# Optimization experiments

Measured on AMD Instinct MI355X. Metric: run time of the kernel, lower is better.

## Reference

```python
import jax, jax.numpy as jnp
import numpy as np

B, LS, LH, D1, D2 = 16, 1024, 1024, 1024, 1024


def setup_inputs() -> dict:
    key = jax.random.key(0)
    k1, k2, k3 = jax.random.split(key, 3)
    S = jax.random.normal(k1, (B, LS, D1), dtype=jnp.float32)
    H = jax.random.normal(k2, (B, LH, D2), dtype=jnp.float32)
    pad_mask = jnp.zeros((B, LS, LH), dtype=jnp.float32)  # additive mask
    W_w = jax.random.normal(k3, (D2, D1), dtype=jnp.float32) / np.sqrt(D1)
    W_b = jnp.zeros((D2,), dtype=jnp.float32)
    return {"S": S, "H": H, "pad_mask": pad_mask, "W_w": W_w, "W_b": W_b}


def reference(S, H, pad_mask, W_w, W_b):
    # Linear projection: S_ = S @ W^T + b  -> [B, LS, D2]
    S_ = jnp.einsum('bsd,ed->bse', S, W_w) + W_b
    # Unscaled dot-product scores: [B, LS, LH]
    score = jnp.einsum('bse,bte->bst', S_, H)
    score = score + pad_mask  # additive pad mask
    score = jax.nn.softmax(score, axis=-1)
    # Weighted sum of H: [B, LS, D2]
    out = jnp.einsum('bst,bte->bse', score, H)
    return out
```

## Files before the change

kernel.cpp:

```cpp
#include <hip/hip_runtime.h>
#include <stdint.h>

typedef _Float16 half8 __attribute__((ext_vector_type(8)));
typedef float floatx4 __attribute__((ext_vector_type(4)));

__device__ __forceinline__ uint16_t f16bits(_Float16 h) {
  union { _Float16 f; uint16_t u; } x; x.f = h; return x.u;
}

__device__ __forceinline__ void g2l16(const void* g, void* l) {
  __builtin_amdgcn_global_load_lds((const __attribute__((address_space(1))) void*)g,
                                   (__attribute__((address_space(3))) void*)l,
                                   16, 0, 0);
}

__global__ __launch_bounds__(256) void split_f16_kernel(
    const float* __restrict__ x, uint16_t* __restrict__ hi,
    uint16_t* __restrict__ lo, int n4) {
  int i = blockIdx.x * 256 + threadIdx.x;
  if (i >= n4) return;
  float4 v = ((const float4*)x)[i];
  ushort4 h, l;
  _Float16 a;
  a = (_Float16)v.x; h.x = f16bits(a); l.x = f16bits((_Float16)(v.x - (float)a));
  a = (_Float16)v.y; h.y = f16bits(a); l.y = f16bits((_Float16)(v.y - (float)a));
  a = (_Float16)v.z; h.z = f16bits(a); l.z = f16bits((_Float16)(v.z - (float)a));
  a = (_Float16)v.w; h.w = f16bits(a); l.w = f16bits((_Float16)(v.w - (float)a));
  ((ushort4*)hi)[i] = h;
  ((ushort4*)lo)[i] = l;
}

__global__ __launch_bounds__(256) void split_h_kernel(
    const float* __restrict__ src, uint16_t* __restrict__ hi,
    uint16_t* __restrict__ lo, uint16_t* __restrict__ ht) {
  __shared__ uint16_t tile[64][65];
  const int e0 = blockIdx.x * 64;
  const int t0 = blockIdx.y * 64;
  const size_t bb = (size_t)blockIdx.z << 20;
  const int r = threadIdx.x >> 4;
  const int c = (threadIdx.x & 15) * 4;
#pragma unroll
  for (int it = 0; it < 4; ++it) {
    const int tr = r + it * 16;
    const size_t idx = bb + (size_t)(t0 + tr) * 1024 + e0 + c;
    float4 v = *(const float4*)(src + idx);
    ushort4 h, l;
    _Float16 a;
    a = (_Float16)v.x; h.x = f16bits(a); l.x = f16bits((_Float16)(v.x - (float)a));
    a = (_Float16)v.y; h.y = f16bits(a); l.y = f16bits((_Float16)(v.y - (float)a));
    a = (_Float16)v.z; h.z = f16bits(a); l.z = f16bits((_Float16)(v.z - (float)a));
    a = (_Float16)v.w; h.w = f16bits(a); l.w = f16bits((_Float16)(v.w - (float)a));
    *(ushort4*)(hi + idx) = h;
    *(ushort4*)(lo + idx) = l;
    tile[c + 0][tr] = h.x;
    tile[c + 1][tr] = h.y;
    tile[c + 2][tr] = h.z;
    tile[c + 3][tr] = h.w;
  }
  __syncthreads();
#pragma unroll
  for (int it = 0; it < 4; ++it) {
    const int er = r + it * 16;
    ushort4 o;
    o.x = tile[er][c + 0];
    o.y = tile[er][c + 1];
    o.z = tile[er][c + 2];
    o.w = tile[er][c + 3];
    *(ushort4*)(ht + bb + (size_t)(e0 + er) * 1024 + t0 + c) = o;
  }
}

template <bool SPLIT, int MODE, int GMAP>
__global__ __launch_bounds__(256, 4) void gemm_bt(
    const uint16_t* __restrict__ Ahi, const uint16_t* __restrict__ Alo,
    const uint16_t* __restrict__ Bhi, const uint16_t* __restrict__ Blo,
    uint16_t* __restrict__ Chi, uint16_t* __restrict__ Clo,
    float* __restrict__ Cf, const float* __restrict__ mask,
    const float* __restrict__ bias, int N, int K,
    long batchA, long batchB, long batchC) {
  constexpr int NBUF = SPLIT ? 2 : 1;
  constexpr int LOI = SPLIT ? 1 : 0;
  __shared__ __align__(16) uint16_t sA[NBUF][128 * 32];
  __shared__ __align__(16) uint16_t sB[NBUF][128 * 32];

  const int tid = threadIdx.x;
  const int lane = tid & 63;
  const int w = tid >> 6;
  const int wr = w >> 1, wc = w & 1;
  const int quad = lane >> 4, l16 = lane & 15;

  int m_t, n_t, z;
  if constexpr (GMAP == 0) {
    m_t = blockIdx.x; n_t = blockIdx.y; z = 0;
  } else {
    z = blockIdx.x; m_t = blockIdx.y >> 3; n_t = blockIdx.y & 7;
  }
  const int m0 = m_t * 128;
  const int n0 = n_t * 128;
  const size_t zA = (size_t)z * batchA;
  const size_t zB = (size_t)z * batchB;
  const size_t zC = (size_t)z * batchC;

  const int r0 = w * 32 + (lane >> 2);
  const int ldc = (((lane & 3) ^ ((lane >> 2) & 3)) * 16);

  const char* gAh0 = (const char*)(Ahi + zA + (size_t)(m0 + r0) * K) + ldc;
  const char* gAh1 = gAh0 + (size_t)16 * K * 2;
  const char* gBh0 = (const char*)(Bhi + zB + (size_t)(n0 + r0) * K) + ldc;
  const char* gBh1 = gBh0 + (size_t)16 * K * 2;
  const char* gAl0 = gAh0; const char* gAl1 = gAh1;
  const char* gBl0 = gBh0; const char* gBl1 = gBh1;
  if constexpr (SPLIT) {
    gAl0 = (const char*)(Alo + zA + (size_t)(m0 + r0) * K) + ldc;
    gAl1 = gAl0 + (size_t)16 * K * 2;
    gBl0 = (const char*)(Blo + zB + (size_t)(n0 + r0) * K) + ldc;
    gBl1 = gBl0 + (size_t)16 * K * 2;
  }
  uint16_t* lA0 = &sA[0][(w * 32) * 32];
  uint16_t* lA1 = &sA[0][(w * 32 + 16) * 32];
  uint16_t* lB0 = &sB[0][(w * 32) * 32];
  uint16_t* lB1 = &sB[0][(w * 32 + 16) * 32];
  uint16_t* lA0l = &sA[LOI][(w * 32) * 32];
  uint16_t* lA1l = &sA[LOI][(w * 32 + 16) * 32];
  uint16_t* lB0l = &sB[LOI][(w * 32) * 32];
  uint16_t* lB1l = &sB[LOI][(w * 32 + 16) * 32];

  const int aoff = (wr * 64 + l16) * 32 + ((quad ^ (l16 & 3)) * 8);
  const int boff = (wc * 64 + l16) * 32 + ((quad ^ (l16 & 3)) * 8);

  floatx4 acc[4][4];
  floatx4 zero = {0.f, 0.f, 0.f, 0.f};
#pragma unroll
  for (int i = 0; i < 4; ++i)
#pragma unroll
    for (int j = 0; j < 4; ++j) acc[i][j] = zero;

  const int nkt = K >> 5;
  for (int kt = 0; kt < nkt; ++kt) {
    const int kb = kt * 64;
    g2l16(gAh0 + kb, lA0);
    g2l16(gAh1 + kb, lA1);
    g2l16(gBh0 + kb, lB0);
    g2l16(gBh1 + kb, lB1);
    if constexpr (SPLIT) {
      g2l16(gAl0 + kb, lA0l);
      g2l16(gAl1 + kb, lA1l);
      g2l16(gBl0 + kb, lB0l);
      g2l16(gBl1 + kb, lB1l);
    }
    __syncthreads();

    half8 fa[4];
#pragma unroll
    for (int i = 0; i < 4; ++i) fa[i] = *(const half8*)&sA[0][aoff + i * 512];
    if constexpr (SPLIT) {
      half8 fbl[4];
#pragma unroll
      for (int j = 0; j < 4; ++j) fbl[j] = *(const half8*)&sB[1][boff + j * 512];
#pragma unroll
      for (int i = 0; i < 4; ++i)
#pragma unroll
        for (int j = 0; j < 4; ++j)
          acc[i][j] = __builtin_amdgcn_mfma_f32_16x16x32_f16(fa[i], fbl[j], acc[i][j], 0, 0, 0);
    }
    half8 fbh[4];
#pragma unroll
    for (int j = 0; j < 4; ++j) fbh[j] = *(const half8*)&sB[0][boff + j * 512];
#pragma unroll
    for (int i = 0; i < 4; ++i)
#pragma unroll
      for (int j = 0; j < 4; ++j)
        acc[i][j] = __builtin_amdgcn_mfma_f32_16x16x32_f16(fa[i], fbh[j], acc[i][j], 0, 0, 0);
    if constexpr (SPLIT) {
      half8 fal[4];
#pragma unroll
      for (int i = 0; i < 4; ++i) fal[i] = *(const half8*)&sA[1][aoff + i * 512];
#pragma unroll
      for (int i = 0; i < 4; ++i)
#pragma unroll
        for (int j = 0; j < 4; ++j)
          acc[i][j] = __builtin_amdgcn_mfma_f32_16x16x32_f16(fal[i], fbh[j], acc[i][j], 0, 0, 0);
    }
    __syncthreads();
  }

  const int crow0 = m0 + wr * 64 + quad * 4;
  const int ccol0 = n0 + wc * 64 + l16;
#pragma unroll
  for (int j = 0; j < 4; ++j) {
    const int col = ccol0 + j * 16;
    float bj = 0.f;
    if constexpr (MODE == 0) bj = bias[col];
#pragma unroll
    for (int i = 0; i < 4; ++i) {
#pragma unroll
      for (int r = 0; r < 4; ++r) {
        const int row = crow0 + i * 16 + r;
        const size_t idx = zC + (size_t)row * N + col;
        float v = acc[i][j][r];
        if constexpr (MODE == 0) {
          v += bj;
          _Float16 h = (_Float16)v;
          Chi[idx] = f16bits(h);
          Clo[idx] = f16bits((_Float16)(v - (float)h));
        } else if constexpr (MODE == 1) {
          Cf[idx] = v + mask[idx];
        } else {
          Cf[idx] = v;
        }
      }
    }
  }
}

__global__ __launch_bounds__(256) void softmax_kernel(
    const float* __restrict__ sc, uint16_t* __restrict__ p) {
  const int row = blockIdx.x;
  const float* x = sc + (size_t)row * 1024;
  const int t = threadIdx.x;
  float4 v = ((const float4*)x)[t];
  float m = fmaxf(fmaxf(v.x, v.y), fmaxf(v.z, v.w));
#pragma unroll
  for (int off = 32; off; off >>= 1) m = fmaxf(m, __shfl_xor(m, off));
  __shared__ float redm[4];
  __shared__ float reds[4];
  const int wv = t >> 6, ln = t & 63;
  if (ln == 0) redm[wv] = m;
  __syncthreads();
  m = fmaxf(fmaxf(redm[0], redm[1]), fmaxf(redm[2], redm[3]));
  float e0 = __expf(v.x - m), e1 = __expf(v.y - m);
  float e2 = __expf(v.z - m), e3 = __expf(v.w - m);
  float s = e0 + e1 + e2 + e3;
#pragma unroll
  for (int off = 32; off; off >>= 1) s += __shfl_xor(s, off);
  if (ln == 0) reds[wv] = s;
  __syncthreads();
  s = reds[0] + reds[1] + reds[2] + reds[3];
  float inv = 1.f / s;
  ushort4 o;
  o.x = f16bits((_Float16)(e0 * inv));
  o.y = f16bits((_Float16)(e1 * inv));
  o.z = f16bits((_Float16)(e2 * inv));
  o.w = f16bits((_Float16)(e3 * inv));
  ((ushort4*)(p + (size_t)row * 1024))[t] = o;
}

__global__ __launch_bounds__(256) void transpose_f16_kernel(
    const float* __restrict__ src, uint16_t* __restrict__ dst) {
  __shared__ uint16_t tile[64][65];
  const int e0 = blockIdx.x * 64;
  const int t0 = blockIdx.y * 64;
  const size_t bb = (size_t)blockIdx.z << 20;
  const int r = threadIdx.x >> 4;
  const int c = (threadIdx.x & 15) * 4;
#pragma unroll
  for (int it = 0; it < 4; ++it) {
    const int tr = r + it * 16;
    float4 v = *(const float4*)(src + bb + (size_t)(t0 + tr) * 1024 + e0 + c);
    tile[c + 0][tr] = f16bits((_Float16)v.x);
    tile[c + 1][tr] = f16bits((_Float16)v.y);
    tile[c + 2][tr] = f16bits((_Float16)v.z);
    tile[c + 3][tr] = f16bits((_Float16)v.w);
  }
  __syncthreads();
#pragma unroll
  for (int it = 0; it < 4; ++it) {
    const int er = r + it * 16;
    ushort4 o;
    o.x = tile[er][c + 0];
    o.y = tile[er][c + 1];
    o.z = tile[er][c + 2];
    o.w = tile[er][c + 3];
    *(ushort4*)(dst + bb + (size_t)(e0 + er) * 1024 + t0 + c) = o;
  }
}

extern "C" void kernel_launch(void* const* d_in, const int* in_sizes, int n_in,
                              void* d_out, int out_size, void* d_ws, size_t ws_size,
                              hipStream_t stream) {
  (void)in_sizes; (void)n_in; (void)out_size;
  const float* S    = (const float*)d_in[0];
  const float* H    = (const float*)d_in[1];
  const float* mask = (const float*)d_in[2];
  const float* Ww   = (const float*)d_in[3];
  const float* Wb   = (const float*)d_in[4];
  float* out = (float*)d_out;
  char* ws = (char*)d_ws;
  const size_t MB = 1024ull * 1024ull;

  uint16_t* Whi  = (uint16_t*)(ws + 0 * MB);
  uint16_t* Wlo  = (uint16_t*)(ws + 2 * MB);
  uint16_t* Pjhi = (uint16_t*)(ws + 4 * MB);
  uint16_t* Pjlo = (uint16_t*)(ws + 36 * MB);
  uint16_t* Hhi  = (uint16_t*)(ws + 68 * MB);
  uint16_t* Hlo  = (uint16_t*)(ws + 100 * MB);
  uint16_t* Shi  = (uint16_t*)(ws + 132 * MB);
  uint16_t* Slo  = (uint16_t*)(ws + 164 * MB);
  float*    SC   = (float*)(ws + 132 * MB);
  uint16_t* PR   = (uint16_t*)(ws + 68 * MB);

  const bool roomy = ws_size >= 229ull * MB;
  uint16_t* HT = roomy ? (uint16_t*)(ws + 196 * MB)
                       : (uint16_t*)(ws + 100 * MB);

  split_f16_kernel<<<16384, 256, 0, stream>>>(S, Shi, Slo, 4 * 1024 * 1024);
  split_f16_kernel<<<1024, 256, 0, stream>>>(Ww, Whi, Wlo, 256 * 1024);
  if (roomy) {
    split_h_kernel<<<dim3(16, 16, 16), 256, 0, stream>>>(H, Hhi, Hlo, HT);
  } else {
    split_f16_kernel<<<16384, 256, 0, stream>>>(H, Hhi, Hlo, 4 * 1024 * 1024);
  }

  gemm_bt<true, 0, 0><<<dim3(128, 8, 1), 256, 0, stream>>>(
      Shi, Slo, Whi, Wlo, Pjhi, Pjlo, nullptr, nullptr, Wb,
      1024, 1024, 0, 0, 0);
  gemm_bt<true, 1, 1><<<dim3(16, 64, 1), 256, 0, stream>>>(
      Pjhi, Pjlo, Hhi, Hlo, nullptr, nullptr, SC, mask, nullptr,
      1024, 1024, 1048576, 1048576, 1048576);
  softmax_kernel<<<16384, 256, 0, stream>>>(SC, PR);
  if (!roomy) {
    transpose_f16_kernel<<<dim3(16, 16, 16), 256, 0, stream>>>(H, HT);
  }
  gemm_bt<false, 2, 1><<<dim3(16, 64, 1), 256, 0, stream>>>(
      PR, nullptr, HT, nullptr, nullptr, nullptr, out, nullptr, nullptr,
      1024, 1024, 1048576, 1048576, 1048576);
}
```

Baseline: 526.1 us.

## Use 256x256 tiles with 8 waves and double-buffered LDS staging in GEMMs

The GEMM kernel moves from 128x128 tiles on 4 waves to 256x256 tiles on 8 waves, with each wave computing a 128x64 sub-tile. Global-to-LDS loads are now double-buffered, so the next K-slice is fetched while the current one is multiplied. The MFMA loop is raised in priority with s_setprio. The aim is more operand reuse per LDS byte and hiding global-load latency. In exchange, each block holds a 128-element accumulator array per thread and up to 128KB of LDS, so occupancy drops to one block per CU and register pressure or spills are a risk. The batched GEMMs launch only 256 blocks.

New measurement: 556.4 us. 1.06x slower.

```diff
diff --git a/kernel.cpp b/kernel.cpp
--- a/kernel.cpp
+++ b/kernel.cpp
@@ -71,7 +71,7 @@
 }
 
 template <bool SPLIT, int MODE, int GMAP>
-__global__ __launch_bounds__(256, 4) void gemm_bt(
+__global__ __launch_bounds__(512, 2) void gemm_bt(
     const uint16_t* __restrict__ Ahi, const uint16_t* __restrict__ Alo,
     const uint16_t* __restrict__ Bhi, const uint16_t* __restrict__ Blo,
     uint16_t* __restrict__ Chi, uint16_t* __restrict__ Clo,
@@ -79,112 +79,108 @@
     const float* __restrict__ bias, int N, int K,
     long batchA, long batchB, long batchC) {
   constexpr int NBUF = SPLIT ? 2 : 1;
-  constexpr int LOI = SPLIT ? 1 : 0;
-  __shared__ __align__(16) uint16_t sA[NBUF][128 * 32];
-  __shared__ __align__(16) uint16_t sB[NBUF][128 * 32];
+  __shared__ __align__(16) uint16_t sA[2][NBUF][256 * 32];
+  __shared__ __align__(16) uint16_t sB[2][NBUF][256 * 32];
 
   const int tid = threadIdx.x;
   const int lane = tid & 63;
   const int w = tid >> 6;
-  const int wr = w >> 1, wc = w & 1;
+  const int wr = w >> 2, wc = w & 3;
   const int quad = lane >> 4, l16 = lane & 15;
 
   int m_t, n_t, z;
   if constexpr (GMAP == 0) {
     m_t = blockIdx.x; n_t = blockIdx.y; z = 0;
   } else {
-    z = blockIdx.x; m_t = blockIdx.y >> 3; n_t = blockIdx.y & 7;
-  }
-  const int m0 = m_t * 128;
-  const int n0 = n_t * 128;
+    z = blockIdx.x; m_t = blockIdx.y >> 2; n_t = blockIdx.y & 3;
+  }
+  const int m0 = m_t * 256;
+  const int n0 = n_t * 256;
   const size_t zA = (size_t)z * batchA;
   const size_t zB = (size_t)z * batchB;
   const size_t zC = (size_t)z * batchC;
 
   const int r0 = w * 32 + (lane >> 2);
   const int ldc = (((lane & 3) ^ ((lane >> 2) & 3)) * 16);
-
-  const char* gAh0 = (const char*)(Ahi + zA + (size_t)(m0 + r0) * K) + ldc;
-  const char* gAh1 = gAh0 + (size_t)16 * K * 2;
-  const char* gBh0 = (const char*)(Bhi + zB + (size_t)(n0 + r0) * K) + ldc;
-  const char* gBh1 = gBh0 + (size_t)16 * K * 2;
-  const char* gAl0 = gAh0; const char* gAl1 = gAh1;
-  const char* gBl0 = gBh0; const char* gBl1 = gBh1;
+  const size_t rowskip = (size_t)16 * K * 2;
+
+  const char* gAh = (const char*)(Ahi + zA + (size_t)(m0 + r0) * K) + ldc;
+  const char* gBh = (const char*)(Bhi + zB + (size_t)(n0 + r0) * K) + ldc;
+  const char* gAl = gAh;
+  const char* gBl = gBh;
   if constexpr (SPLIT) {
-    gAl0 = (const char*)(Alo + zA + (size_t)(m0 + r0) * K) + ldc;
-    gAl1 = gAl0 + (size_t)16 * K * 2;
-    gBl0 = (const char*)(Blo + zB + (size_t)(n0 + r0) * K) + ldc;
-    gBl1 = gBl0 + (size_t)16 * K * 2;
-  }
-  uint16_t* lA0 = &sA[0][(w * 32) * 32];
-  uint16_t* lA1 = &sA[0][(w * 32 + 16) * 32];
-  uint16_t* lB0 = &sB[0][(w * 32) * 32];
-  uint16_t* lB1 = &sB[0][(w * 32 + 16) * 32];
-  uint16_t* lA0l = &sA[LOI][(w * 32) * 32];
-  uint16_t* lA1l = &sA[LOI][(w * 32 + 16) * 32];
-  uint16_t* lB0l = &sB[LOI][(w * 32) * 32];
-  uint16_t* lB1l = &sB[LOI][(w * 32 + 16) * 32];
-
-  const int aoff = (wr * 64 + l16) * 32 + ((quad ^ (l16 & 3)) * 8);
+    gAl = (const char*)(Alo + zA + (size_t)(m0 + r0) * K) + ldc;
+    gBl = (const char*)(Blo + zB + (size_t)(n0 + r0) * K) + ldc;
+  }
+
+  auto stage = [&](int buf, int kb) {
+    g2l16(gAh + kb, &sA[buf][0][(w * 32) * 32]);
+    g2l16(gAh + rowskip + kb, &sA[buf][0][(w * 32 + 16) * 32]);
+    g2l16(gBh + kb, &sB[buf][0][(w * 32) * 32]);
+    g2l16(gBh + rowskip + kb, &sB[buf][0][(w * 32 + 16) * 32]);
+    if constexpr (SPLIT) {
+      g2l16(gAl + kb, &sA[buf][NBUF - 1][(w * 32) * 32]);
+      g2l16(gAl + rowskip + kb, &sA[buf][NBUF - 1][(w * 32 + 16) * 32]);
+      g2l16(gBl + kb, &sB[buf][NBUF - 1][(w * 32) * 32]);
+      g2l16(gBl + rowskip + kb, &sB[buf][NBUF - 1][(w * 32 + 16) * 32]);
+    }
+  };
+
+  const int aoff = (wr * 128 + l16) * 32 + ((quad ^ (l16 & 3)) * 8);
   const int boff = (wc * 64 + l16) * 32 + ((quad ^ (l16 & 3)) * 8);
 
-  floatx4 acc[4][4];
+  floatx4 acc[8][4];
   floatx4 zero = {0.f, 0.f, 0.f, 0.f};
 #pragma unroll
-  for (int i = 0; i < 4; ++i)
+  for (int i = 0; i < 8; ++i)
 #pragma unroll
     for (int j = 0; j < 4; ++j) acc[i][j] = zero;
 
   const int nkt = K >> 5;
+  stage(0, 0);
+  __syncthreads();
+  int cur = 0;
   for (int kt = 0; kt < nkt; ++kt) {
-    const int kb = kt * 64;
-    g2l16(gAh0 + kb, lA0);
-    g2l16(gAh1 + kb, lA1);
-    g2l16(gBh0 + kb, lB0);
-    g2l16(gBh1 + kb, lB1);
+    if (kt + 1 < nkt) stage(cur ^ 1, (kt + 1) * 64);
+
+    const uint16_t* pAh = &sA[cur][0][0];
+    const uint16_t* pBh = &sB[cur][0][0];
+    const uint16_t* pAl = &sA[cur][NBUF - 1][0];
+    const uint16_t* pBl = &sB[cur][NBUF - 1][0];
+    half8 fbh[4], fbl[4];
     if constexpr (SPLIT) {
-      g2l16(gAl0 + kb, lA0l);
-      g2l16(gAl1 + kb, lA1l);
-      g2l16(gBl0 + kb, lB0l);
-      g2l16(gBl1 + kb, lB1l);
+#pragma unroll
+      for (int j = 0; j < 4; ++j) fbl[j] = *(const half8*)&pBl[boff + j * 512];
     }
+#pragma unroll
+    for (int j = 0; j < 4; ++j) fbh[j] = *(const half8*)&pBh[boff + j * 512];
+    __builtin_amdgcn_s_setprio(1);
+#pragma unroll
+    for (int i = 0; i < 8; ++i) {
+      half8 fah = *(const half8*)&pAh[aoff + i * 512];
+      if constexpr (SPLIT) {
+        half8 fal = *(const half8*)&pAl[aoff + i * 512];
+#pragma unroll
+        for (int j = 0; j < 4; ++j)
+          acc[i][j] = __builtin_amdgcn_mfma_f32_16x16x32_f16(fah, fbl[j], acc[i][j], 0, 0, 0);
+#pragma unroll
+        for (int j = 0; j < 4; ++j)
+          acc[i][j] = __builtin_amdgcn_mfma_f32_16x16x32_f16(fah, fbh[j], acc[i][j], 0, 0, 0);
+#pragma unroll
+        for (int j = 0; j < 4; ++j)
+          acc[i][j] = __builtin_amdgcn_mfma_f32_16x16x32_f16(fal, fbh[j], acc[i][j], 0, 0, 0);
+      } else {
+#pragma unroll
+        for (int j = 0; j < 4; ++j)
+          acc[i][j] = __builtin_amdgcn_mfma_f32_16x16x32_f16(fah, fbh[j], acc[i][j], 0, 0, 0);
+      }
+    }
+    __builtin_amdgcn_s_setprio(0);
     __syncthreads();
-
-    half8 fa[4];
-#pragma unroll
-    for (int i = 0; i < 4; ++i) fa[i] = *(const half8*)&sA[0][aoff + i * 512];
-    if constexpr (SPLIT) {
-      half8 fbl[4];
-#pragma unroll
-      for (int j = 0; j < 4; ++j) fbl[j] = *(const half8*)&sB[1][boff + j * 512];
-#pragma unroll
-      for (int i = 0; i < 4; ++i)
-#pragma unroll
-        for (int j = 0; j < 4; ++j)
-          acc[i][j] = __builtin_amdgcn_mfma_f32_16x16x32_f16(fa[i], fbl[j], acc[i][j], 0, 0, 0);
-    }
-    half8 fbh[4];
-#pragma unroll
-    for (int j = 0; j < 4; ++j) fbh[j] = *(const half8*)&sB[0][boff + j * 512];
-#pragma unroll
-    for (int i = 0; i < 4; ++i)
-#pragma unroll
-      for (int j = 0; j < 4; ++j)
-        acc[i][j] = __builtin_amdgcn_mfma_f32_16x16x32_f16(fa[i], fbh[j], acc[i][j], 0, 0, 0);
-    if constexpr (SPLIT) {
-      half8 fal[4];
-#pragma unroll
-      for (int i = 0; i < 4; ++i) fal[i] = *(const half8*)&sA[1][aoff + i * 512];
-#pragma unroll
-      for (int i = 0; i < 4; ++i)
-#pragma unroll
-        for (int j = 0; j < 4; ++j)
-          acc[i][j] = __builtin_amdgcn_mfma_f32_16x16x32_f16(fal[i], fbh[j], acc[i][j], 0, 0, 0);
-    }
-    __syncthreads();
-  }
-
-  const int crow0 = m0 + wr * 64 + quad * 4;
+    cur ^= 1;
+  }
+
+  const int crow0 = m0 + wr * 128 + quad * 4;
   const int ccol0 = n0 + wc * 64 + l16;
 #pragma unroll
   for (int j = 0; j < 4; ++j) {
@@ -192,7 +188,7 @@
     float bj = 0.f;
     if constexpr (MODE == 0) bj = bias[col];
 #pragma unroll
-    for (int i = 0; i < 4; ++i) {
+    for (int i = 0; i < 8; ++i) {
 #pragma unroll
       for (int r = 0; r < 4; ++r) {
         const int row = crow0 + i * 16 + r;
@@ -311,17 +307,17 @@
     split_f16_kernel<<<16384, 256, 0, stream>>>(H, Hhi, Hlo, 4 * 1024 * 1024);
   }
 
-  gemm_bt<true, 0, 0><<<dim3(128, 8, 1), 256, 0, stream>>>(
+  gemm_bt<true, 0, 0><<<dim3(64, 4, 1), 512, 0, stream>>>(
       Shi, Slo, Whi, Wlo, Pjhi, Pjlo, nullptr, nullptr, Wb,
       1024, 1024, 0, 0, 0);
-  gemm_bt<true, 1, 1><<<dim3(16, 64, 1), 256, 0, stream>>>(
+  gemm_bt<true, 1, 1><<<dim3(16, 16, 1), 512, 0, stream>>>(
       Pjhi, Pjlo, Hhi, Hlo, nullptr, nullptr, SC, mask, nullptr,
       1024, 1024, 1048576, 1048576, 1048576);
   softmax_kernel<<<16384, 256, 0, stream>>>(SC, PR);
   if (!roomy) {
     transpose_f16_kernel<<<dim3(16, 16, 16), 256, 0, stream>>>(H, HT);
   }
-  gemm_bt<false, 2, 1><<<dim3(16, 64, 1), 256, 0, stream>>>(
+  gemm_bt<false, 2, 1><<<dim3(16, 16, 1), 512, 0, stream>>>(
       PR, nullptr, HT, nullptr, nullptr, nullptr, out, nullptr, nullptr,
       1024, 1024, 1048576, 1048576, 1048576);
 }
```

## Double-buffer LDS tiles in gemm_bt to overlap global loads with MFMA

Applied to the files above, without the earlier changes.

Adds a second LDS buffer for the A/B tiles in the GEMM kernel. The next K-tile is prefetched through global_load_lds while MFMAs run on the current one, and the per-iteration barriers drop from two to one. This is meant to hide global-memory latency behind compute. The cost is double the shared memory: the split (hi/lo) variant grows to about 64KB per block, which may lower the number of resident blocks per CU below the launch-bounds target of 4.

Result: faster. 506.3 us (-3.8%).

```diff
diff --git a/kernel.cpp b/kernel.cpp
--- a/kernel.cpp
+++ b/kernel.cpp
@@ -80,8 +80,8 @@
     long batchA, long batchB, long batchC) {
   constexpr int NBUF = SPLIT ? 2 : 1;
   constexpr int LOI = SPLIT ? 1 : 0;
-  __shared__ __align__(16) uint16_t sA[NBUF][128 * 32];
-  __shared__ __align__(16) uint16_t sB[NBUF][128 * 32];
+  __shared__ __align__(16) uint16_t sA[2][NBUF][128 * 32];
+  __shared__ __align__(16) uint16_t sB[2][NBUF][128 * 32];
 
   const int tid = threadIdx.x;
   const int lane = tid & 63;
@@ -116,14 +116,20 @@
     gBl0 = (const char*)(Blo + zB + (size_t)(n0 + r0) * K) + ldc;
     gBl1 = gBl0 + (size_t)16 * K * 2;
   }
-  uint16_t* lA0 = &sA[0][(w * 32) * 32];
-  uint16_t* lA1 = &sA[0][(w * 32 + 16) * 32];
-  uint16_t* lB0 = &sB[0][(w * 32) * 32];
-  uint16_t* lB1 = &sB[0][(w * 32 + 16) * 32];
-  uint16_t* lA0l = &sA[LOI][(w * 32) * 32];
-  uint16_t* lA1l = &sA[LOI][(w * 32 + 16) * 32];
-  uint16_t* lB0l = &sB[LOI][(w * 32) * 32];
-  uint16_t* lB1l = &sB[LOI][(w * 32 + 16) * 32];
+
+  auto stage = [&](int buf, int kt) {
+    const int kb = kt * 64;
+    g2l16(gAh0 + kb, &sA[buf][0][(w * 32) * 32]);
+    g2l16(gAh1 + kb, &sA[buf][0][(w * 32 + 16) * 32]);
+    g2l16(gBh0 + kb, &sB[buf][0][(w * 32) * 32]);
+    g2l16(gBh1 + kb, &sB[buf][0][(w * 32 + 16) * 32]);
+    if constexpr (SPLIT) {
+      g2l16(gAl0 + kb, &sA[buf][LOI][(w * 32) * 32]);
+      g2l16(gAl1 + kb, &sA[buf][LOI][(w * 32 + 16) * 32]);
+      g2l16(gBl0 + kb, &sB[buf][LOI][(w * 32) * 32]);
+      g2l16(gBl1 + kb, &sB[buf][LOI][(w * 32 + 16) * 32]);
+    }
+  };
 
   const int aoff = (wr * 64 + l16) * 32 + ((quad ^ (l16 & 3)) * 8);
   const int boff = (wc * 64 + l16) * 32 + ((quad ^ (l16 & 3)) * 8);
@@ -136,27 +142,19 @@
     for (int j = 0; j < 4; ++j) acc[i][j] = zero;
 
   const int nkt = K >> 5;
+  stage(0, 0);
+  __syncthreads();
+  int cur = 0;
   for (int kt = 0; kt < nkt; ++kt) {
-    const int kb = kt * 64;
-    g2l16(gAh0 + kb, lA0);
-    g2l16(gAh1 + kb, lA1);
-    g2l16(gBh0 + kb, lB0);
-    g2l16(gBh1 + kb, lB1);
-    if constexpr (SPLIT) {
-      g2l16(gAl0 + kb, lA0l);
-      g2l16(gAl1 + kb, lA1l);
-      g2l16(gBl0 + kb, lB0l);
-      g2l16(gBl1 + kb, lB1l);
-    }
-    __syncthreads();
+    if (kt + 1 < nkt) stage(cur ^ 1, kt + 1);
 
     half8 fa[4];
 #pragma unroll
-    for (int i = 0; i < 4; ++i) fa[i] = *(const half8*)&sA[0][aoff + i * 512];
+    for (int i = 0; i < 4; ++i) fa[i] = *(const half8*)&sA[cur][0][aoff + i * 512];
     if constexpr (SPLIT) {
       half8 fbl[4];
 #pragma unroll
-      for (int j = 0; j < 4; ++j) fbl[j] = *(const half8*)&sB[1][boff + j * 512];
+      for (int j = 0; j < 4; ++j) fbl[j] = *(const half8*)&sB[cur][1][boff + j * 512];
 #pragma unroll
       for (int i = 0; i < 4; ++i)
 #pragma unroll
@@ -165,7 +163,7 @@
     }
     half8 fbh[4];
 #pragma unroll
-    for (int j = 0; j < 4; ++j) fbh[j] = *(const half8*)&sB[0][boff + j * 512];
+    for (int j = 0; j < 4; ++j) fbh[j] = *(const half8*)&sB[cur][0][boff + j * 512];
 #pragma unroll
     for (int i = 0; i < 4; ++i)
 #pragma unroll
@@ -174,7 +172,7 @@
     if constexpr (SPLIT) {
       half8 fal[4];
 #pragma unroll
-      for (int i = 0; i < 4; ++i) fal[i] = *(const half8*)&sA[1][aoff + i * 512];
+      for (int i = 0; i < 4; ++i) fal[i] = *(const half8*)&sA[cur][1][aoff + i * 512];
 #pragma unroll
       for (int i = 0; i < 4; ++i)
 #pragma unroll
@@ -182,6 +180,7 @@
           acc[i][j] = __builtin_amdgcn_mfma_f32_16x16x32_f16(fal[i], fbh[j], acc[i][j], 0, 0, 0);
     }
     __syncthreads();
+    cur ^= 1;
   }
 
   const int crow0 = m0 + wr * 64 + quad * 4;
```
